# Kernel optimization log

Hardware: AMD Instinct MI355X
Metric: run time of the kernel (lower is better)

## Reference

```python
import jax, jax.numpy as jnp
import numpy as np

C = 768
HEADS = 12

def setup_inputs() -> dict:
    key = jax.random.key(0)
    k1, k2, k3 = jax.random.split(key, 3)
    x = jax.random.normal(k1, (8, C, 32, 32), dtype=jnp.float32)
    # 1x1 convs are channel-wise linear maps; store as [out_c, in_c]
    w_qkv = jax.random.normal(k2, (3 * C, C), dtype=jnp.float32) * (C ** -0.5)
    w_proj = jax.random.normal(k3, (C, C), dtype=jnp.float32) * (C ** -0.5)
    return {"x": x, "w_qkv": w_qkv, "w_proj": w_proj}

def reference(x, w_qkv, w_proj):
    b, c, h, w = x.shape
    heads = HEADS
    dh = c // heads
    n = h * w
    scale = dh ** -0.5
    # 1x1 conv QKV: [b, 3c, h, w] -> [b, 3, heads, dh, n]
    qkv = jnp.einsum('oc,bchw->bohw', w_qkv, x).reshape(b, 3, heads, dh, n)
    q, k, v = qkv[:, 0], qkv[:, 1], qkv[:, 2]  # each [b, heads, dh, n]
    attn = jnp.einsum('bhdn,bhdm->bhnm', q, k) * scale  # [b, heads, n, n]
    attn = jax.nn.softmax(attn, axis=-1)
    out = jnp.einsum('bhnm,bhdm->bhdn', attn, v)  # [b, heads, dh, n]
    out = out.reshape(b, c, h, w)
    return jnp.einsum('oc,bchw->bohw', w_proj, out)
```

## Files before the change

### kernel.cpp

```cpp
#include <hip/hip_runtime.h>

typedef unsigned short u16;
typedef unsigned int u32;
typedef float v4f __attribute__((ext_vector_type(4)));
typedef __bf16 bf16x8 __attribute__((ext_vector_type(8)));

#define BATCH 8
#define CDIM 768
#define NHEAD 12
#define DH 64
#define NSEQ 1024
#define SCL 0.18033688011112042f

__device__ __forceinline__ u16 f2bf(float f) {
  u32 u = __builtin_bit_cast(u32, f);
  u += 0x7fffu + ((u >> 16) & 1u);
  return (u16)(u >> 16);
}

__device__ __forceinline__ v4f mfma16(bf16x8 a, bf16x8 b, v4f c) {
  return __builtin_amdgcn_mfma_f32_16x16x32_bf16(a, b, c, 0, 0, 0);
}

__device__ __forceinline__ void gload16(const u16* g, u16* l) {
  __builtin_amdgcn_global_load_lds(
      (const __attribute__((address_space(1))) void*)g,
      (__attribute__((address_space(3))) void*)l, 16, 0, 0);
}

__global__ __launch_bounds__(256) void k_conv(const float* __restrict__ s,
                                              u16* __restrict__ d, int n4) {
  int i = blockIdx.x * 256 + threadIdx.x;
  if (i < n4) {
    float4 v = ((const float4*)s)[i];
    u32 lo = (u32)f2bf(v.x) | ((u32)f2bf(v.y) << 16);
    u32 hi = (u32)f2bf(v.z) | ((u32)f2bf(v.w) << 16);
    ((uint2*)d)[i] = uint2{lo, hi};
  }
}

__global__ __launch_bounds__(256) void k_transpose(const float* __restrict__ x,
                                                   u16* __restrict__ xT) {
  int b = blockIdx.z, c0 = blockIdx.y * 64, p0 = blockIdx.x * 64;
  __shared__ u16 Ts[64][72];
  int t = threadIdx.x;
  int cr = t >> 4;
  int p4 = (t & 15) * 4;
  const float* src = x + ((size_t)b * CDIM + c0) * NSEQ + p0;
#pragma unroll
  for (int i = 0; i < 4; ++i) {
    int c = cr + i * 16;
    float4 v = *(const float4*)&src[(size_t)c * NSEQ + p4];
    Ts[p4 + 0][c] = f2bf(v.x);
    Ts[p4 + 1][c] = f2bf(v.y);
    Ts[p4 + 2][c] = f2bf(v.z);
    Ts[p4 + 3][c] = f2bf(v.w);
  }
  __syncthreads();
  int p = t >> 2;
  int cq = t & 3;
  u16* dst = xT + ((size_t)b * NSEQ + p0 + p) * CDIM + c0;
#pragma unroll
  for (int j = 0; j < 2; ++j) {
    int ch = cq + j * 4;
    *(int4*)&dst[ch * 8] = *(const int4*)&Ts[p][ch * 8];
  }
}

__global__ __launch_bounds__(256) void k_gemm_qkv(const u16* __restrict__ Wb,
                                                  const u16* __restrict__ xT,
                                                  u16* __restrict__ qkT,
                                                  u16* __restrict__ vbuf) {
  int b = blockIdx.x, oT = blockIdx.y * 128, pT = blockIdx.z * 128;
  __shared__ u16 As[128 * 32];
  __shared__ u16 Bs[128 * 32];
  int t = threadIdx.x, lane = t & 63, wid = t >> 6;
  int ln = lane & 15, quad = lane >> 4;
  int wr = wid >> 1, wc = wid & 1;
  v4f acc[4][4] = {};

  int lr = lane >> 2, lc = (lane & 3) * 8;
  const u16* Ag = Wb + (size_t)(oT + wid * 16 + lr) * CDIM + lc;
  const u16* Bg = xT + ((size_t)b * NSEQ + pT + wid * 16 + lr) * CDIM + lc;
  u16* Asl = &As[(wid * 16) * 32];
  u16* Asl2 = &As[(wid * 16 + 64) * 32];
  u16* Bsl = &Bs[(wid * 16) * 32];
  u16* Bsl2 = &Bs[(wid * 16 + 64) * 32];

  for (int kk = 0; kk < CDIM; kk += 32) {
    gload16(Ag + kk, Asl);
    gload16(Ag + (size_t)64 * CDIM + kk, Asl2);
    gload16(Bg + kk, Bsl);
    gload16(Bg + (size_t)64 * CDIM + kk, Bsl2);
    __syncthreads();
    bf16x8 af[4], bfr[4];
#pragma unroll
    for (int mt = 0; mt < 4; ++mt)
      af[mt] = *(const bf16x8*)&As[(wr * 64 + mt * 16 + ln) * 32 + quad * 8];
#pragma unroll
    for (int nt = 0; nt < 4; ++nt)
      bfr[nt] = *(const bf16x8*)&Bs[(wc * 64 + nt * 16 + ln) * 32 + quad * 8];
#pragma unroll
    for (int mt = 0; mt < 4; ++mt)
#pragma unroll
      for (int nt = 0; nt < 4; ++nt)
        acc[mt][nt] = mfma16(af[mt], bfr[nt], acc[mt][nt]);
    __syncthreads();
  }

  bool isV = (oT >= 2 * CDIM);
#pragma unroll
  for (int mt = 0; mt < 4; ++mt) {
#pragma unroll
    for (int nt = 0; nt < 4; ++nt) {
      int ro = oT + wr * 64 + mt * 16 + quad * 4;
      int cp = pT + wc * 64 + nt * 16 + ln;
      if (!isV) {
        u32 lo = (u32)f2bf(acc[mt][nt][0]) | ((u32)f2bf(acc[mt][nt][1]) << 16);
        u32 hi = (u32)f2bf(acc[mt][nt][2]) | ((u32)f2bf(acc[mt][nt][3]) << 16);
        *(uint2*)&qkT[((size_t)b * NSEQ + cp) * 1536 + ro] = uint2{lo, hi};
      } else {
#pragma unroll
        for (int r = 0; r < 4; ++r)
          vbuf[((size_t)b * CDIM + (ro - 2 * CDIM + r)) * NSEQ + cp] =
              f2bf(acc[mt][nt][r]);
      }
    }
  }
}

__global__ __launch_bounds__(512) void k_attn(const u16* __restrict__ qkT,
                                              const u16* __restrict__ vbuf,
                                              u16* __restrict__ attnT) {
  int id = blockIdx.x;
  int b = id & 7;
  int j = id >> 3;
  int ntile = j & 3;
  int h = j >> 2;
  int nt0 = ntile * 256;

  int t = threadIdx.x, lane = t & 63, wid = t >> 6;
  int ln = lane & 15, quad = lane >> 4;
  int nbase = nt0 + wid * 32;

  __shared__ u16 Ks[64 * 72];
  __shared__ u16 Vs[64 * 72];
  __shared__ u16 Pa[8][32 * 72];
  u16* myP = Pa[wid];

  const u16* qbase = qkT + ((size_t)b * NSEQ + nbase) * 1536 + h * DH;
  bf16x8 aq[2][2];
#pragma unroll
  for (int mt = 0; mt < 2; ++mt)
#pragma unroll
    for (int ks = 0; ks < 2; ++ks)
      aq[mt][ks] = *(const bf16x8*)&qbase[(size_t)(mt * 16 + ln) * 1536 + ks * 32 + quad * 8];

  v4f oacc[2][4] = {};
  float lsum[2] = {0.0f, 0.0f};

  const u16* kg0 = qkT + (size_t)b * NSEQ * 1536 + CDIM + h * DH;
  const u16* vg0 = vbuf + ((size_t)b * CDIM + h * DH) * NSEQ;
  int sr = t >> 3;
  int sc = (t & 7) * 8;

  for (int m0 = 0; m0 < NSEQ; m0 += 64) {
    __syncthreads();
    *(int4*)&Ks[sr * 72 + sc] = *(const int4*)(kg0 + (size_t)(m0 + sr) * 1536 + sc);
    *(int4*)&Vs[sr * 72 + sc] = *(const int4*)(vg0 + (size_t)sr * NSEQ + m0 + sc);
    __syncthreads();

#pragma unroll
    for (int ct = 0; ct < 4; ++ct) {
      bf16x8 kf0 = *(const bf16x8*)&Ks[(ct * 16 + ln) * 72 + quad * 8];
      bf16x8 kf1 = *(const bf16x8*)&Ks[(ct * 16 + ln) * 72 + 32 + quad * 8];
#pragma unroll
      for (int mt = 0; mt < 2; ++mt) {
        v4f s = {};
        s = mfma16(kf0, aq[mt][0], s);
        s = mfma16(kf1, aq[mt][1], s);
        float p0 = __builtin_amdgcn_exp2f(s[0] * SCL);
        float p1 = __builtin_amdgcn_exp2f(s[1] * SCL);
        float p2 = __builtin_amdgcn_exp2f(s[2] * SCL);
        float p3 = __builtin_amdgcn_exp2f(s[3] * SCL);
        lsum[mt] += (p0 + p1) + (p2 + p3);
        u32 lo = (u32)f2bf(p0) | ((u32)f2bf(p1) << 16);
        u32 hi = (u32)f2bf(p2) | ((u32)f2bf(p3) << 16);
        *(uint2*)&myP[(mt * 16 + ln) * 72 + ct * 16 + quad * 4] = uint2{lo, hi};
      }
    }

    bf16x8 ap[2][2];
#pragma unroll
    for (int mt = 0; mt < 2; ++mt)
#pragma unroll
      for (int ks = 0; ks < 2; ++ks)
        ap[mt][ks] = *(const bf16x8*)&myP[(mt * 16 + ln) * 72 + ks * 32 + quad * 8];
#pragma unroll
    for (int nt = 0; nt < 4; ++nt) {
      bf16x8 vf0 = *(const bf16x8*)&Vs[(nt * 16 + ln) * 72 + quad * 8];
      bf16x8 vf1 = *(const bf16x8*)&Vs[(nt * 16 + ln) * 72 + 32 + quad * 8];
#pragma unroll
      for (int mt = 0; mt < 2; ++mt) {
        oacc[mt][nt] = mfma16(ap[mt][0], vf0, oacc[mt][nt]);
        oacc[mt][nt] = mfma16(ap[mt][1], vf1, oacc[mt][nt]);
      }
    }
  }

#pragma unroll
  for (int mt = 0; mt < 2; ++mt) {
    lsum[mt] += __shfl_xor(lsum[mt], 16);
    lsum[mt] += __shfl_xor(lsum[mt], 32);
  }

#pragma unroll
  for (int mt = 0; mt < 2; ++mt) {
#pragma unroll
    for (int r = 0; r < 4; ++r) {
      float l = __shfl(lsum[mt], quad * 4 + r, 16);
      float inv = 1.0f / l;
      int n = nbase + mt * 16 + quad * 4 + r;
      u16* dst = attnT + ((size_t)b * NSEQ + n) * CDIM + h * DH;
#pragma unroll
      for (int nt = 0; nt < 4; ++nt)
        dst[nt * 16 + ln] = f2bf(oacc[mt][nt][r] * inv);
    }
  }
}

__global__ __launch_bounds__(256) void k_gemm_proj(const u16* __restrict__ Wb,
                                                   const u16* __restrict__ aT,
                                                   float* __restrict__ out) {
  int b = blockIdx.x, oT = blockIdx.y * 128, pT = blockIdx.z * 128;
  __shared__ u16 As[128 * 32];
  __shared__ u16 Bs[128 * 32];
  int t = threadIdx.x, lane = t & 63, wid = t >> 6;
  int ln = lane & 15, quad = lane >> 4;
  int wr = wid >> 1, wc = wid & 1;
  v4f acc[4][4] = {};

  int lr = lane >> 2, lc = (lane & 3) * 8;
  const u16* Ag = Wb + (size_t)(oT + wid * 16 + lr) * CDIM + lc;
  const u16* Bg = aT + ((size_t)b * NSEQ + pT + wid * 16 + lr) * CDIM + lc;
  u16* Asl = &As[(wid * 16) * 32];
  u16* Asl2 = &As[(wid * 16 + 64) * 32];
  u16* Bsl = &Bs[(wid * 16) * 32];
  u16* Bsl2 = &Bs[(wid * 16 + 64) * 32];

  for (int kk = 0; kk < CDIM; kk += 32) {
    gload16(Ag + kk, Asl);
    gload16(Ag + (size_t)64 * CDIM + kk, Asl2);
    gload16(Bg + kk, Bsl);
    gload16(Bg + (size_t)64 * CDIM + kk, Bsl2);
    __syncthreads();
    bf16x8 af[4], bfr[4];
#pragma unroll
    for (int mt = 0; mt < 4; ++mt)
      af[mt] = *(const bf16x8*)&As[(wr * 64 + mt * 16 + ln) * 32 + quad * 8];
#pragma unroll
    for (int nt = 0; nt < 4; ++nt)
      bfr[nt] = *(const bf16x8*)&Bs[(wc * 64 + nt * 16 + ln) * 32 + quad * 8];
#pragma unroll
    for (int mt = 0; mt < 4; ++mt)
#pragma unroll
      for (int nt = 0; nt < 4; ++nt)
        acc[mt][nt] = mfma16(af[mt], bfr[nt], acc[mt][nt]);
    __syncthreads();
  }

#pragma unroll
  for (int mt = 0; mt < 4; ++mt) {
#pragma unroll
    for (int nt = 0; nt < 4; ++nt) {
      int ro = oT + wr * 64 + mt * 16 + quad * 4;
      int cp = pT + wc * 64 + nt * 16 + ln;
#pragma unroll
      for (int r = 0; r < 4; ++r)
        out[((size_t)b * CDIM + ro + r) * NSEQ + cp] = acc[mt][nt][r];
    }
  }
}

extern "C" void kernel_launch(void* const* d_in, const int* in_sizes, int n_in,
                              void* d_out, int out_size, void* d_ws, size_t ws_size,
                              hipStream_t stream) {
  const float* x = (const float*)d_in[0];
  const float* w_qkv = (const float*)d_in[1];
  const float* w_proj = (const float*)d_in[2];
  float* out = (float*)d_out;

  char* ws = (char*)d_ws;
  u16* wqkv_bf = (u16*)(ws);
  u16* wproj_bf = (u16*)(ws + 3538944);
  u16* xT = (u16*)(ws + 4718592);
  u16* vbuf = (u16*)(ws + 17301504);
  u16* qkT = (u16*)d_out;
  u16* attnT = xT;

  k_conv<<<dim3(1728), dim3(256), 0, stream>>>(w_qkv, wqkv_bf, 442368);
  k_conv<<<dim3(576), dim3(256), 0, stream>>>(w_proj, wproj_bf, 147456);
  k_transpose<<<dim3(16, 12, 8), dim3(256), 0, stream>>>(x, xT);
  k_gemm_qkv<<<dim3(8, 18, 8), dim3(256), 0, stream>>>(wqkv_bf, xT, qkT, vbuf);
  k_attn<<<dim3(384), dim3(512), 0, stream>>>(qkT, vbuf, attnT);
  k_gemm_proj<<<dim3(8, 6, 8), dim3(256), 0, stream>>>(wproj_bf, attnT, out);
}
```

Before: 209.0 us.

## Fuse prep kernels and double-buffer the QKV GEMM global-to-LDS loads

The two weight-conversion kernels and the input transpose are merged into one launch that uses block-index ranges to split the work. The QKV GEMM now double-buffers its LDS tiles, prefetching the next K slice while computing on the current one. It uses explicit vmcnt waits and raw barriers in place of __syncthreads. The grid is also reordered so the output-channel tile varies fastest, which changes how blocks share input tiles in cache. This removes two launches and hides global-load latency, but it doubles LDS use and relies on hand-written waitcnt encodings being correct.

```diff
diff --git a/kernel.cpp b/kernel.cpp
--- a/kernel.cpp
+++ b/kernel.cpp
@@ -12,6 +12,9 @@
 #define NSEQ 1024
 #define SCL 0.18033688011112042f
 
+#define WAIT_VM4 0xF74
+#define WAIT_VM0 0xF70
+
 __device__ __forceinline__ u16 f2bf(float f) {
   u32 u = __builtin_bit_cast(u32, f);
   u += 0x7fffu + ((u >> 16) & 1u);
@@ -28,22 +31,29 @@
       (__attribute__((address_space(3))) void*)l, 16, 0, 0);
 }
 
-__global__ __launch_bounds__(256) void k_conv(const float* __restrict__ s,
-                                              u16* __restrict__ d, int n4) {
-  int i = blockIdx.x * 256 + threadIdx.x;
-  if (i < n4) {
+__global__ __launch_bounds__(256) void k_prep(const float* __restrict__ x,
+                                              const float* __restrict__ wq,
+                                              const float* __restrict__ wp,
+                                              u16* __restrict__ xT,
+                                              u16* __restrict__ wqb,
+                                              u16* __restrict__ wpb) {
+  __shared__ u16 Ts[64][72];
+  int bid = blockIdx.x;
+  int t = threadIdx.x;
+  if (bid < 2304) {
+    bool isQ = bid < 1728;
+    const float* s = isQ ? wq : wp;
+    u16* d = isQ ? wqb : wpb;
+    int i = (isQ ? bid : bid - 1728) * 256 + t;
     float4 v = ((const float4*)s)[i];
     u32 lo = (u32)f2bf(v.x) | ((u32)f2bf(v.y) << 16);
     u32 hi = (u32)f2bf(v.z) | ((u32)f2bf(v.w) << 16);
     ((uint2*)d)[i] = uint2{lo, hi};
-  }
-}
-
-__global__ __launch_bounds__(256) void k_transpose(const float* __restrict__ x,
-                                                   u16* __restrict__ xT) {
-  int b = blockIdx.z, c0 = blockIdx.y * 64, p0 = blockIdx.x * 64;
-  __shared__ u16 Ts[64][72];
-  int t = threadIdx.x;
+    return;
+  }
+  int id = bid - 2304;
+  int p0 = (id & 15) * 64; id >>= 4;
+  int c0 = (id % 12) * 64; int b = id / 12;
   int cr = t >> 4;
   int p4 = (t & 15) * 4;
   const float* src = x + ((size_t)b * CDIM + c0) * NSEQ + p0;
@@ -71,9 +81,9 @@
                                                   const u16* __restrict__ xT,
                                                   u16* __restrict__ qkT,
                                                   u16* __restrict__ vbuf) {
-  int b = blockIdx.x, oT = blockIdx.y * 128, pT = blockIdx.z * 128;
-  __shared__ u16 As[128 * 32];
-  __shared__ u16 Bs[128 * 32];
+  int oT = blockIdx.x * 128, pT = blockIdx.y * 128, b = blockIdx.z;
+  __shared__ u16 As[2][128 * 32];
+  __shared__ u16 Bs[2][128 * 32];
   int t = threadIdx.x, lane = t & 63, wid = t >> 6;
   int ln = lane & 15, quad = lane >> 4;
   int wr = wid >> 1, wc = wid & 1;
@@ -82,30 +92,40 @@
   int lr = lane >> 2, lc = (lane & 3) * 8;
   const u16* Ag = Wb + (size_t)(oT + wid * 16 + lr) * CDIM + lc;
   const u16* Bg = xT + ((size_t)b * NSEQ + pT + wid * 16 + lr) * CDIM + lc;
-  u16* Asl = &As[(wid * 16) * 32];
-  u16* Asl2 = &As[(wid * 16 + 64) * 32];
-  u16* Bsl = &Bs[(wid * 16) * 32];
-  u16* Bsl2 = &Bs[(wid * 16 + 64) * 32];
-
-  for (int kk = 0; kk < CDIM; kk += 32) {
-    gload16(Ag + kk, Asl);
-    gload16(Ag + (size_t)64 * CDIM + kk, Asl2);
-    gload16(Bg + kk, Bsl);
-    gload16(Bg + (size_t)64 * CDIM + kk, Bsl2);
-    __syncthreads();
+  int s0 = (wid * 16) * 32, s1 = (wid * 16 + 64) * 32;
+
+  gload16(Ag, &As[0][s0]);
+  gload16(Ag + (size_t)64 * CDIM, &As[0][s1]);
+  gload16(Bg, &Bs[0][s0]);
+  gload16(Bg + (size_t)64 * CDIM, &Bs[0][s1]);
+
+#pragma unroll 2
+  for (int k = 0; k < 24; ++k) {
+    int cur = k & 1, nxt = cur ^ 1;
+    if (k < 23) {
+      int kk = (k + 1) * 32;
+      gload16(Ag + kk, &As[nxt][s0]);
+      gload16(Ag + (size_t)64 * CDIM + kk, &As[nxt][s1]);
+      gload16(Bg + kk, &Bs[nxt][s0]);
+      gload16(Bg + (size_t)64 * CDIM + kk, &Bs[nxt][s1]);
+      __builtin_amdgcn_s_waitcnt(WAIT_VM4);
+    } else {
+      __builtin_amdgcn_s_waitcnt(WAIT_VM0);
+    }
+    __builtin_amdgcn_s_barrier();
     bf16x8 af[4], bfr[4];
 #pragma unroll
     for (int mt = 0; mt < 4; ++mt)
-      af[mt] = *(const bf16x8*)&As[(wr * 64 + mt * 16 + ln) * 32 + quad * 8];
+      af[mt] = *(const bf16x8*)&As[cur][(wr * 64 + mt * 16 + ln) * 32 + quad * 8];
 #pragma unroll
     for (int nt = 0; nt < 4; ++nt)
-      bfr[nt] = *(const bf16x8*)&Bs[(wc * 64 + nt * 16 + ln) * 32 + quad * 8];
+      bfr[nt] = *(const bf16x8*)&Bs[cur][(wc * 64 + nt * 16 + ln) * 32 + quad * 8];
 #pragma unroll
     for (int mt = 0; mt < 4; ++mt)
 #pragma unroll
       for (int nt = 0; nt < 4; ++nt)
         acc[mt][nt] = mfma16(af[mt], bfr[nt], acc[mt][nt]);
-    __syncthreads();
+    __builtin_amdgcn_s_barrier();
   }
 
   bool isV = (oT >= 2 * CDIM);
@@ -298,10 +318,8 @@
   u16* qkT = (u16*)d_out;
   u16* attnT = xT;
 
-  k_conv<<<dim3(1728), dim3(256), 0, stream>>>(w_qkv, wqkv_bf, 442368);
-  k_conv<<<dim3(576), dim3(256), 0, stream>>>(w_proj, wproj_bf, 147456);
-  k_transpose<<<dim3(16, 12, 8), dim3(256), 0, stream>>>(x, xT);
-  k_gemm_qkv<<<dim3(8, 18, 8), dim3(256), 0, stream>>>(wqkv_bf, xT, qkT, vbuf);
+  k_prep<<<dim3(3840), dim3(256), 0, stream>>>(x, w_qkv, w_proj, xT, wqkv_bf, wproj_bf);
+  k_gemm_qkv<<<dim3(18, 8, 8), dim3(256), 0, stream>>>(wqkv_bf, xT, qkT, vbuf);
   k_attn<<<dim3(384), dim3(512), 0, stream>>>(qkT, vbuf, attnT);
   k_gemm_proj<<<dim3(8, 6, 8), dim3(256), 0, stream>>>(wproj_bf, attnT, out);
 }
```

New measurement: 206.6 us. About the same (-1.1%).
